# Kernel tuning notes

Hardware: AMD Instinct MI355X
Metric: run time of the kernel (lower is better)

The kernel has to match this reference:

```python
import jax, jax.numpy as jnp
import numpy as np

N_NODES = 100000


def gcn_conv(x, edge_index, W, b, num_nodes):
    """PyG GCNConv: y = D^{-1/2} (A + I) D^{-1/2} (x W) + b.

    edge_index[0] = source (row), edge_index[1] = target (col);
    messages flow source -> target with symmetric normalization.
    """
    # add self loops
    loop = jnp.arange(num_nodes, dtype=edge_index.dtype)
    row = jnp.concatenate([edge_index[0], loop])  # [E+N]
    col = jnp.concatenate([edge_index[1], loop])  # [E+N]

    xw = x @ W  # [N, F_out] -- tiny GEMM, done before gather

    # degree of target nodes (incl. self loops)
    ones = jnp.ones(col.shape[0], dtype=x.dtype)
    deg = jax.ops.segment_sum(ones, col, num_segments=num_nodes)  # [N]
    dis = jax.lax.rsqrt(jnp.maximum(deg, 1e-12))
    dis = jnp.where(deg > 0, dis, 0.0)

    norm = dis[row] * dis[col]  # [E+N]
    msg = xw[row] * norm[:, None]  # gather + scale, [E+N, F_out]
    out = jax.ops.segment_sum(msg, col, num_segments=num_nodes)  # scatter-add
    return out + b


def setup_inputs() -> dict:
    key = jax.random.key(0)
    k1, k2, k3, k4 = jax.random.split(key, 4)
    num_attr, hidden, num_classes = 128, 16, 8
    n_edges = 3200000
    x = jax.random.normal(k1, (N_NODES, num_attr), dtype=jnp.float32)
    edge_index = jax.random.randint(k2, (2, n_edges), 0, N_NODES, dtype=jnp.int64)
    W1 = jax.random.normal(k3, (num_attr, hidden), dtype=jnp.float32) / np.sqrt(num_attr)
    b1 = jnp.zeros((hidden,), dtype=jnp.float32)
    W2 = jax.random.normal(k4, (hidden, num_classes), dtype=jnp.float32) / np.sqrt(hidden)
    b2 = jnp.zeros((num_classes,), dtype=jnp.float32)
    return {"x": x, "edge_index": edge_index, "W1": W1, "b1": b1, "W2": W2, "b2": b2}


def reference(x, edge_index, W1, b1, W2, b2):
    h = gcn_conv(x, edge_index, W1, b1, N_NODES)
    h = jax.nn.relu(h)
    # dropout is identity in eval mode
    h = gcn_conv(h, edge_index, W2, b2, N_NODES)
    return jax.nn.sigmoid(h)  # [N, num_classes]
```

## Files before the change

kernel.cpp:

```cpp
#include <hip/hip_runtime.h>
#include <math.h>

static constexpr int FI = 128;
static constexpr int FH = 16;
static constexpr int FO = 8;

static constexpr int BIN_SHIFT = 10;
static constexpr int BIN_NODES = 1024;
static constexpr int MAX_BINS  = 128;
static constexpr int CAPB      = 35328;
static constexpr int SCHUNK    = 4096;
static constexpr int SThreads  = 512;

__device__ __forceinline__ unsigned short f2bf(float x) {
    unsigned u = __float_as_uint(x);
    u += 0x7FFFu + ((u >> 16) & 1u);
    return (unsigned short)(u >> 16);
}
__device__ __forceinline__ float bf2f(unsigned short h) {
    return __uint_as_float((unsigned)h << 16);
}
__device__ __forceinline__ float bflo(unsigned u) { return __uint_as_float(u << 16); }
__device__ __forceinline__ float bfhi(unsigned u) { return __uint_as_float(u & 0xFFFF0000u); }

__global__ void k_initcur(int* __restrict__ binCursor, int nbins) {
    int i = threadIdx.x;
    if (i < nbins) binCursor[i] = i * CAPB;
}

__launch_bounds__(SThreads)
__global__ void k_binscatter(const int* __restrict__ row, const int* __restrict__ col,
                             int* __restrict__ binCursor, unsigned int* __restrict__ binned,
                             int E, int nbins) {
    __shared__ int lcnt[MAX_BINS];
    __shared__ int lsc[MAX_BINS];
    __shared__ int lstart[MAX_BINS];
    __shared__ int lcur[MAX_BINS];
    __shared__ int gbase[MAX_BINS];
    __shared__ unsigned int  staged[SCHUNK];
    __shared__ unsigned char sbin[SCHUNK];
    int t = threadIdx.x;
    int base = blockIdx.x * SCHUNK;
    int end  = base + SCHUNK; if (end > E) end = E;
    int m = end - base;
    if (t < MAX_BINS) lcnt[t] = 0;
    __syncthreads();

    int nv = m >> 2;
    const int4* c4 = (const int4*)(col + base);
    for (int k = t; k < nv; k += SThreads) {
        int4 c = c4[k];
        atomicAdd(&lcnt[c.x >> BIN_SHIFT], 1);
        atomicAdd(&lcnt[c.y >> BIN_SHIFT], 1);
        atomicAdd(&lcnt[c.z >> BIN_SHIFT], 1);
        atomicAdd(&lcnt[c.w >> BIN_SHIFT], 1);
    }
    for (int i = base + (nv << 2) + t; i < end; i += SThreads)
        atomicAdd(&lcnt[col[i] >> BIN_SHIFT], 1);
    __syncthreads();

    int v = 0;
    if (t < MAX_BINS) { v = lcnt[t]; lsc[t] = v; }
    __syncthreads();
    for (int off = 1; off < MAX_BINS; off <<= 1) {
        int x = (t >= off && t < MAX_BINS) ? lsc[t - off] : 0;
        __syncthreads();
        if (t < MAX_BINS) lsc[t] += x;
        __syncthreads();
    }
    if (t < MAX_BINS) {
        int ex = lsc[t] - v;
        lstart[t] = ex;
        lcur[t]   = ex;
        gbase[t]  = v ? atomicAdd(&binCursor[t], v) : 0;
    }
    __syncthreads();

    const int4* r4 = (const int4*)(row + base);
    for (int k = t; k < nv; k += SThreads) {
        int4 c = c4[k]; int4 r = r4[k];
        int cc[4] = {c.x, c.y, c.z, c.w};
        int rr[4] = {r.x, r.y, r.z, r.w};
        #pragma unroll
        for (int j = 0; j < 4; ++j) {
            int b = cc[j] >> BIN_SHIFT;
            int pos = atomicAdd(&lcur[b], 1);
            staged[pos] = (unsigned)rr[j] | ((unsigned)(cc[j] & (BIN_NODES - 1)) << 17);
            sbin[pos] = (unsigned char)b;
        }
    }
    for (int i = base + (nv << 2) + t; i < end; i += SThreads) {
        int c = col[i];
        int b = c >> BIN_SHIFT;
        int pos = atomicAdd(&lcur[b], 1);
        staged[pos] = (unsigned)row[i] | ((unsigned)(c & (BIN_NODES - 1)) << 17);
        sbin[pos] = (unsigned char)b;
    }
    __syncthreads();

    for (int i = t; i < m; i += SThreads) {
        int b = sbin[i];
        int g = gbase[b] + (i - lstart[b]);
        if (g < (b + 1) * CAPB) binned[g] = staged[i];
    }
}

__launch_bounds__(1024)
__global__ void k_refine(const int* __restrict__ binCursor, const unsigned int* __restrict__ binned,
                         int* __restrict__ srow, int* __restrict__ starts, int* __restrict__ ends,
                         float* __restrict__ dis, int N) {
    __shared__ int cnt[BIN_NODES];
    __shared__ int ls[BIN_NODES];
    int t = threadIdx.x;
    int b = blockIdx.x;
    int s = b * CAPB;
    int m = binCursor[b] - s;
    if (m > CAPB) m = CAPB;
    cnt[t] = 0;
    __syncthreads();

    int mm = m & ~3;
    for (int i0 = t * 4; i0 < mm; i0 += 4096) {
        uint4 v = *(const uint4*)(binned + s + i0);
        atomicAdd(&cnt[v.x >> 17], 1);
        atomicAdd(&cnt[v.y >> 17], 1);
        atomicAdd(&cnt[v.z >> 17], 1);
        atomicAdd(&cnt[v.w >> 17], 1);
    }
    for (int i = mm + t; i < m; i += 1024)
        atomicAdd(&cnt[binned[s + i] >> 17], 1);
    __syncthreads();

    int deg = cnt[t];
    ls[t] = deg;
    __syncthreads();
    for (int off = 1; off < 1024; off <<= 1) {
        int x = (t >= off) ? ls[t - off] : 0;
        __syncthreads();
        ls[t] += x;
        __syncthreads();
    }
    int excl = ls[t] - deg;

    int n = b * BIN_NODES + t;
    if (n < N) {
        starts[n] = s + excl;
        ends[n]   = s + excl + deg;
        dis[n]    = rsqrtf((float)(deg + 1));
    }
    cnt[t] = excl;
    __syncthreads();

    for (int i0 = t * 4; i0 < mm; i0 += 4096) {
        uint4 v = *(const uint4*)(binned + s + i0);
        int p0 = atomicAdd(&cnt[v.x >> 17], 1); srow[s + p0] = v.x & 0x1FFFF;
        int p1 = atomicAdd(&cnt[v.y >> 17], 1); srow[s + p1] = v.y & 0x1FFFF;
        int p2 = atomicAdd(&cnt[v.z >> 17], 1); srow[s + p2] = v.z & 0x1FFFF;
        int p3 = atomicAdd(&cnt[v.w >> 17], 1); srow[s + p3] = v.w & 0x1FFFF;
    }
    for (int i = mm + t; i < m; i += 1024) {
        unsigned v = binned[s + i];
        int p = atomicAdd(&cnt[v >> 17], 1);
        srow[s + p] = v & 0x1FFFF;
    }
}

__launch_bounds__(256)
__global__ void k_gemm1(const float* __restrict__ x, const float* __restrict__ W,
                        const float* __restrict__ dis, unsigned short* __restrict__ xw1s,
                        int N) {
    __shared__ float sw[FI * FH];
    int t = threadIdx.x;
    for (int i = t; i < FI * FH; i += 256) sw[i] = W[i];
    __syncthreads();

    int nl = t >> 2;
    int f  = (t & 3) * 4;
    int n  = blockIdx.x * 64 + nl;
    if (n >= N) return;

    const float4* xr = (const float4*)(x + (size_t)n * FI);
    float a0 = 0.f, a1 = 0.f, a2 = 0.f, a3 = 0.f;
    #pragma unroll 8
    for (int kq = 0; kq < FI / 4; ++kq) {
        float4 xv = xr[kq];
        float4 w0 = *(const float4*)&sw[(kq * 4 + 0) * FH + f];
        float4 w1 = *(const float4*)&sw[(kq * 4 + 1) * FH + f];
        float4 w2 = *(const float4*)&sw[(kq * 4 + 2) * FH + f];
        float4 w3 = *(const float4*)&sw[(kq * 4 + 3) * FH + f];
        a0 = fmaf(xv.x, w0.x, a0); a1 = fmaf(xv.x, w0.y, a1);
        a2 = fmaf(xv.x, w0.z, a2); a3 = fmaf(xv.x, w0.w, a3);
        a0 = fmaf(xv.y, w1.x, a0); a1 = fmaf(xv.y, w1.y, a1);
        a2 = fmaf(xv.y, w1.z, a2); a3 = fmaf(xv.y, w1.w, a3);
        a0 = fmaf(xv.z, w2.x, a0); a1 = fmaf(xv.z, w2.y, a1);
        a2 = fmaf(xv.z, w2.z, a2); a3 = fmaf(xv.z, w2.w, a3);
        a0 = fmaf(xv.w, w3.x, a0); a1 = fmaf(xv.w, w3.y, a1);
        a2 = fmaf(xv.w, w3.z, a2); a3 = fmaf(xv.w, w3.w, a3);
    }
    float dn = dis[n];
    unsigned w0 = (unsigned)f2bf(a0 * dn) | ((unsigned)f2bf(a1 * dn) << 16);
    unsigned w1 = (unsigned)f2bf(a2 * dn) | ((unsigned)f2bf(a3 * dn) << 16);
    *(uint2*)(xw1s + (size_t)n * FH + f) = make_uint2(w0, w1);
}

__launch_bounds__(256)
__global__ void k_agg1(const int* __restrict__ starts, const int* __restrict__ ends,
                       const int* __restrict__ srow, const float* __restrict__ dis,
                       const unsigned short* __restrict__ xw1s, const float* __restrict__ W2,
                       const float* __restrict__ b1, unsigned short* __restrict__ xw2s, int N) {
    __shared__ float h1[64][FH + 1];
    __shared__ float sw[FH * FO];
    __shared__ float sb[FH];
    int t = threadIdx.x;
    if (t < FH * FO) sw[t] = W2[t];
    if (t < FH) sb[t] = b1[t];
    int nl = t >> 2;
    int q  = t & 3;
    int n  = blockIdx.x * 64 + nl;
    float dn = 0.f;
    if (n < N) {
        dn = dis[n];
        int s = starts[n], e = ends[n];
        const uint2* xq = (const uint2*)(xw1s) + q;
        uint2 selfpk = xq[(size_t)n * 4];
        float a0 = bflo(selfpk.x), a1 = bfhi(selfpk.x);
        float a2 = bflo(selfpk.y), a3 = bfhi(selfpk.y);
        int i = s;
        for (; i + 8 <= e; i += 8) {
            int rr[8];
            #pragma unroll
            for (int j = 0; j < 8; ++j) rr[j] = srow[i + j];
            uint2 pk[8];
            #pragma unroll
            for (int j = 0; j < 8; ++j) pk[j] = xq[(size_t)rr[j] * 4];
            #pragma unroll
            for (int j = 0; j < 8; ++j) {
                a0 += bflo(pk[j].x); a1 += bfhi(pk[j].x);
                a2 += bflo(pk[j].y); a3 += bfhi(pk[j].y);
            }
        }
        for (; i < e; ++i) {
            uint2 p = xq[(size_t)srow[i] * 4];
            a0 += bflo(p.x); a1 += bfhi(p.x);
            a2 += bflo(p.y); a3 += bfhi(p.y);
        }
        int f0 = q * 4;
        float v0 = fmaf(dn, a0, sb[f0 + 0]);
        float v1 = fmaf(dn, a1, sb[f0 + 1]);
        float v2 = fmaf(dn, a2, sb[f0 + 2]);
        float v3 = fmaf(dn, a3, sb[f0 + 3]);
        h1[nl][f0 + 0] = v0 > 0.f ? v0 : 0.f;
        h1[nl][f0 + 1] = v1 > 0.f ? v1 : 0.f;
        h1[nl][f0 + 2] = v2 > 0.f ? v2 : 0.f;
        h1[nl][f0 + 3] = v3 > 0.f ? v3 : 0.f;
    }
    __syncthreads();
    if (n < N) {
        int o0 = q * 2;
        float aL = 0.f, aH = 0.f;
        #pragma unroll
        for (int k = 0; k < FH; ++k) {
            float hv = h1[nl][k];
            aL = fmaf(hv, sw[k * FO + o0],     aL);
            aH = fmaf(hv, sw[k * FO + o0 + 1], aH);
        }
        unsigned pk = (unsigned)f2bf(aL * dn) | ((unsigned)f2bf(aH * dn) << 16);
        *(unsigned*)(xw2s + (size_t)n * FO + o0) = pk;
    }
}

__launch_bounds__(256)
__global__ void k_agg2(const int* __restrict__ starts, const int* __restrict__ ends,
                       const int* __restrict__ srow, const float* __restrict__ dis,
                       const unsigned short* __restrict__ xw2s, const float* __restrict__ b2,
                       float* __restrict__ out, int N) {
    int t = threadIdx.x;
    int nl = t >> 1;
    int h  = t & 1;
    int n  = blockIdx.x * 128 + nl;
    if (n >= N) return;
    float dn = dis[n];
    int s = starts[n], e = ends[n];
    const uint2* xq = (const uint2*)(xw2s) + h;
    uint2 selfpk = xq[(size_t)n * 2];
    float a0 = bflo(selfpk.x), a1 = bfhi(selfpk.x);
    float a2 = bflo(selfpk.y), a3 = bfhi(selfpk.y);
    int i = s;
    for (; i + 8 <= e; i += 8) {
        int rr[8];
        #pragma unroll
        for (int j = 0; j < 8; ++j) rr[j] = srow[i + j];
        uint2 pk[8];
        #pragma unroll
        for (int j = 0; j < 8; ++j) pk[j] = xq[(size_t)rr[j] * 2];
        #pragma unroll
        for (int j = 0; j < 8; ++j) {
            a0 += bflo(pk[j].x); a1 += bfhi(pk[j].x);
            a2 += bflo(pk[j].y); a3 += bfhi(pk[j].y);
        }
    }
    for (; i < e; ++i) {
        uint2 p = xq[(size_t)srow[i] * 2];
        a0 += bflo(p.x); a1 += bfhi(p.x);
        a2 += bflo(p.y); a3 += bfhi(p.y);
    }
    int f0 = h * 4;
    float v0 = fmaf(dn, a0, b2[f0 + 0]);
    float v1 = fmaf(dn, a1, b2[f0 + 1]);
    float v2 = fmaf(dn, a2, b2[f0 + 2]);
    float v3 = fmaf(dn, a3, b2[f0 + 3]);
    float4 r = make_float4(1.f / (1.f + __expf(-v0)), 1.f / (1.f + __expf(-v1)),
                           1.f / (1.f + __expf(-v2)), 1.f / (1.f + __expf(-v3)));
    *(float4*)(out + (size_t)n * FO + f0) = r;
}

extern "C" void kernel_launch(void* const* d_in, const int* in_sizes, int n_in,
                              void* d_out, int out_size, void* d_ws, size_t ws_size,
                              hipStream_t stream) {
    const float* x  = (const float*)d_in[0];
    const int*   ei = (const int*)d_in[1];
    const float* W1 = (const float*)d_in[2];
    const float* b1 = (const float*)d_in[3];
    const float* W2 = (const float*)d_in[4];
    const float* b2 = (const float*)d_in[5];

    const int N = in_sizes[0] / FI;
    const int E = in_sizes[1] / 2;
    const int* row = ei;
    const int* col = ei + E;
    const int nbins = (N + BIN_NODES - 1) >> BIN_SHIFT;

    const size_t NP = 100352;
    const size_t BINSZ = (size_t)nbins * CAPB;
    float* base = (float*)d_ws;
    int*   starts    = (int*)base;
    int*   ends      = (int*)(base + NP);
    float* dis       = base + 2 * NP;
    int*   binCursor = (int*)(base + 3 * NP);
    unsigned int* binned = (unsigned int*)(base + 3 * NP + 1024);
    int*   srow      = (int*)(base + 3 * NP + 1024 + BINSZ);
    unsigned short* xw1s = (unsigned short*)binned;
    unsigned short* xw2s = (unsigned short*)(base + 3 * NP + 1024 + NP * 8);
    float* out = (float*)d_out;

    size_t needed = (3 * NP + 1024 + 2 * BINSZ) * 4;
    if (ws_size < needed) return;

    k_initcur   <<<1, 128,                               0, stream>>>(binCursor, nbins);
    k_binscatter<<<(E + SCHUNK - 1) / SCHUNK, SThreads,  0, stream>>>(row, col, binCursor, binned, E, nbins);
    k_refine    <<<nbins, 1024,                          0, stream>>>(binCursor, binned, srow, starts, ends, dis, N);
    k_gemm1     <<<(N + 63) / 64, 256,                   0, stream>>>(x, W1, dis, xw1s, N);
    k_agg1      <<<(N + 63) / 64, 256,                   0, stream>>>(starts, ends, srow, dis, xw1s, W2, b1, xw2s, N);
    k_agg2      <<<(N + 127) / 128, 256,                 0, stream>>>(starts, ends, srow, dis, xw2s, b2, out, N);
}
```

Measured before the change: 134.6 us.

## Use one thread per node in aggregation kernels and wave-shuffle scan in refine

Both aggregation kernels now assign a whole node to a single thread, which loads the full bf16 feature row with 16-byte vector loads instead of splitting features across 2-4 threads. This cuts the repeated index loads and the shared-memory transpose for the second GEMM, at the cost of more registers and fewer threads per node for latency hiding. The refine kernel's 10-step shared-memory prefix scan becomes a wave-level shuffle scan plus a small cross-wave pass. The binscatter chunk size is also doubled.

```diff
diff --git a/kernel.cpp b/kernel.cpp
--- a/kernel.cpp
+++ b/kernel.cpp
@@ -9,16 +9,13 @@
 static constexpr int BIN_NODES = 1024;
 static constexpr int MAX_BINS  = 128;
 static constexpr int CAPB      = 35328;
-static constexpr int SCHUNK    = 4096;
+static constexpr int SCHUNK    = 8192;
 static constexpr int SThreads  = 512;
 
 __device__ __forceinline__ unsigned short f2bf(float x) {
     unsigned u = __float_as_uint(x);
     u += 0x7FFFu + ((u >> 16) & 1u);
     return (unsigned short)(u >> 16);
-}
-__device__ __forceinline__ float bf2f(unsigned short h) {
-    return __uint_as_float((unsigned)h << 16);
 }
 __device__ __forceinline__ float bflo(unsigned u) { return __uint_as_float(u << 16); }
 __device__ __forceinline__ float bfhi(unsigned u) { return __uint_as_float(u & 0xFFFF0000u); }
@@ -110,7 +107,7 @@
                          int* __restrict__ srow, int* __restrict__ starts, int* __restrict__ ends,
                          float* __restrict__ dis, int N) {
     __shared__ int cnt[BIN_NODES];
-    __shared__ int ls[BIN_NODES];
+    __shared__ int wsum[16];
     int t = threadIdx.x;
     int b = blockIdx.x;
     int s = b * CAPB;
@@ -132,15 +129,26 @@
     __syncthreads();
 
     int deg = cnt[t];
-    ls[t] = deg;
-    __syncthreads();
-    for (int off = 1; off < 1024; off <<= 1) {
-        int x = (t >= off) ? ls[t - off] : 0;
-        __syncthreads();
-        ls[t] += x;
-        __syncthreads();
-    }
-    int excl = ls[t] - deg;
+    int inc = deg;
+    #pragma unroll
+    for (int d = 1; d < 64; d <<= 1) {
+        int u = __shfl_up(inc, d, 64);
+        if ((t & 63) >= d) inc += u;
+    }
+    if ((t & 63) == 63) wsum[t >> 6] = inc;
+    __syncthreads();
+    if (t < 16) {
+        int w = wsum[t];
+        #pragma unroll
+        for (int d = 1; d < 16; d <<= 1) {
+            int u = __shfl_up(w, d, 16);
+            if (t >= d) w += u;
+        }
+        wsum[t] = w;
+    }
+    __syncthreads();
+    int waveoff = (t >= 64) ? wsum[(t >> 6) - 1] : 0;
+    int excl = waveoff + inc - deg;
 
     int n = b * BIN_NODES + t;
     if (n < N) {
@@ -208,65 +216,80 @@
                        const int* __restrict__ srow, const float* __restrict__ dis,
                        const unsigned short* __restrict__ xw1s, const float* __restrict__ W2,
                        const float* __restrict__ b1, unsigned short* __restrict__ xw2s, int N) {
-    __shared__ float h1[64][FH + 1];
     __shared__ float sw[FH * FO];
     __shared__ float sb[FH];
     int t = threadIdx.x;
     if (t < FH * FO) sw[t] = W2[t];
     if (t < FH) sb[t] = b1[t];
-    int nl = t >> 2;
-    int q  = t & 3;
-    int n  = blockIdx.x * 64 + nl;
-    float dn = 0.f;
-    if (n < N) {
-        dn = dis[n];
-        int s = starts[n], e = ends[n];
-        const uint2* xq = (const uint2*)(xw1s) + q;
-        uint2 selfpk = xq[(size_t)n * 4];
-        float a0 = bflo(selfpk.x), a1 = bfhi(selfpk.x);
-        float a2 = bflo(selfpk.y), a3 = bfhi(selfpk.y);
-        int i = s;
-        for (; i + 8 <= e; i += 8) {
-            int rr[8];
-            #pragma unroll
-            for (int j = 0; j < 8; ++j) rr[j] = srow[i + j];
-            uint2 pk[8];
-            #pragma unroll
-            for (int j = 0; j < 8; ++j) pk[j] = xq[(size_t)rr[j] * 4];
-            #pragma unroll
-            for (int j = 0; j < 8; ++j) {
-                a0 += bflo(pk[j].x); a1 += bfhi(pk[j].x);
-                a2 += bflo(pk[j].y); a3 += bfhi(pk[j].y);
-            }
-        }
-        for (; i < e; ++i) {
-            uint2 p = xq[(size_t)srow[i] * 4];
-            a0 += bflo(p.x); a1 += bfhi(p.x);
-            a2 += bflo(p.y); a3 += bfhi(p.y);
-        }
-        int f0 = q * 4;
-        float v0 = fmaf(dn, a0, sb[f0 + 0]);
-        float v1 = fmaf(dn, a1, sb[f0 + 1]);
-        float v2 = fmaf(dn, a2, sb[f0 + 2]);
-        float v3 = fmaf(dn, a3, sb[f0 + 3]);
-        h1[nl][f0 + 0] = v0 > 0.f ? v0 : 0.f;
-        h1[nl][f0 + 1] = v1 > 0.f ? v1 : 0.f;
-        h1[nl][f0 + 2] = v2 > 0.f ? v2 : 0.f;
-        h1[nl][f0 + 3] = v3 > 0.f ? v3 : 0.f;
-    }
-    __syncthreads();
-    if (n < N) {
-        int o0 = q * 2;
+    __syncthreads();
+
+    int n = blockIdx.x * 256 + t;
+    if (n >= N) return;
+    float dn = dis[n];
+    int s = starts[n], e = ends[n];
+    const uint4* xq = (const uint4*)xw1s;
+
+    uint4 s0 = xq[(size_t)n * 2], s1 = xq[(size_t)n * 2 + 1];
+    float acc[16];
+    acc[0]=bflo(s0.x); acc[1]=bfhi(s0.x); acc[2]=bflo(s0.y); acc[3]=bfhi(s0.y);
+    acc[4]=bflo(s0.z); acc[5]=bfhi(s0.z); acc[6]=bflo(s0.w); acc[7]=bfhi(s0.w);
+    acc[8]=bflo(s1.x); acc[9]=bfhi(s1.x); acc[10]=bflo(s1.y); acc[11]=bfhi(s1.y);
+    acc[12]=bflo(s1.z); acc[13]=bfhi(s1.z); acc[14]=bflo(s1.w); acc[15]=bfhi(s1.w);
+
+    int i = s;
+    for (; i + 8 <= e; i += 8) {
+        int rr[8];
+        #pragma unroll
+        for (int j = 0; j < 8; ++j) rr[j] = srow[i + j];
+        uint4 pa[8], pb[8];
+        #pragma unroll
+        for (int j = 0; j < 8; ++j) {
+            pa[j] = xq[(size_t)rr[j] * 2];
+            pb[j] = xq[(size_t)rr[j] * 2 + 1];
+        }
+        #pragma unroll
+        for (int j = 0; j < 8; ++j) {
+            acc[0]+=bflo(pa[j].x);  acc[1]+=bfhi(pa[j].x);
+            acc[2]+=bflo(pa[j].y);  acc[3]+=bfhi(pa[j].y);
+            acc[4]+=bflo(pa[j].z);  acc[5]+=bfhi(pa[j].z);
+            acc[6]+=bflo(pa[j].w);  acc[7]+=bfhi(pa[j].w);
+            acc[8]+=bflo(pb[j].x);  acc[9]+=bfhi(pb[j].x);
+            acc[10]+=bflo(pb[j].y); acc[11]+=bfhi(pb[j].y);
+            acc[12]+=bflo(pb[j].z); acc[13]+=bfhi(pb[j].z);
+            acc[14]+=bflo(pb[j].w); acc[15]+=bfhi(pb[j].w);
+        }
+    }
+    for (; i < e; ++i) {
+        int r = srow[i];
+        uint4 qa = xq[(size_t)r * 2], qb = xq[(size_t)r * 2 + 1];
+        acc[0]+=bflo(qa.x);  acc[1]+=bfhi(qa.x);
+        acc[2]+=bflo(qa.y);  acc[3]+=bfhi(qa.y);
+        acc[4]+=bflo(qa.z);  acc[5]+=bfhi(qa.z);
+        acc[6]+=bflo(qa.w);  acc[7]+=bfhi(qa.w);
+        acc[8]+=bflo(qb.x);  acc[9]+=bfhi(qb.x);
+        acc[10]+=bflo(qb.y); acc[11]+=bfhi(qb.y);
+        acc[12]+=bflo(qb.z); acc[13]+=bfhi(qb.z);
+        acc[14]+=bflo(qb.w); acc[15]+=bfhi(qb.w);
+    }
+
+    float hv[FH];
+    #pragma unroll
+    for (int k = 0; k < FH; ++k) {
+        float v = fmaf(dn, acc[k], sb[k]);
+        hv[k] = v > 0.f ? v : 0.f;
+    }
+    unsigned o[4];
+    #pragma unroll
+    for (int p = 0; p < 4; ++p) {
         float aL = 0.f, aH = 0.f;
         #pragma unroll
         for (int k = 0; k < FH; ++k) {
-            float hv = h1[nl][k];
-            aL = fmaf(hv, sw[k * FO + o0],     aL);
-            aH = fmaf(hv, sw[k * FO + o0 + 1], aH);
-        }
-        unsigned pk = (unsigned)f2bf(aL * dn) | ((unsigned)f2bf(aH * dn) << 16);
-        *(unsigned*)(xw2s + (size_t)n * FO + o0) = pk;
-    }
+            aL = fmaf(hv[k], sw[k * FO + 2 * p],     aL);
+            aH = fmaf(hv[k], sw[k * FO + 2 * p + 1], aH);
+        }
+        o[p] = (unsigned)f2bf(aL * dn) | ((unsigned)f2bf(aH * dn) << 16);
+    }
+    *(uint4*)(xw2s + (size_t)n * FO) = make_uint4(o[0], o[1], o[2], o[3]);
 }
 
 __launch_bounds__(256)
@@ -275,43 +298,49 @@
                        const unsigned short* __restrict__ xw2s, const float* __restrict__ b2,
                        float* __restrict__ out, int N) {
     int t = threadIdx.x;
-    int nl = t >> 1;
-    int h  = t & 1;
-    int n  = blockIdx.x * 128 + nl;
+    int n = blockIdx.x * 256 + t;
     if (n >= N) return;
     float dn = dis[n];
     int s = starts[n], e = ends[n];
-    const uint2* xq = (const uint2*)(xw2s) + h;
-    uint2 selfpk = xq[(size_t)n * 2];
-    float a0 = bflo(selfpk.x), a1 = bfhi(selfpk.x);
-    float a2 = bflo(selfpk.y), a3 = bfhi(selfpk.y);
+    const uint4* xq = (const uint4*)xw2s;
+
+    uint4 sp = xq[n];
+    float acc[8];
+    acc[0]=bflo(sp.x); acc[1]=bfhi(sp.x); acc[2]=bflo(sp.y); acc[3]=bfhi(sp.y);
+    acc[4]=bflo(sp.z); acc[5]=bfhi(sp.z); acc[6]=bflo(sp.w); acc[7]=bfhi(sp.w);
+
     int i = s;
     for (; i + 8 <= e; i += 8) {
         int rr[8];
         #pragma unroll
         for (int j = 0; j < 8; ++j) rr[j] = srow[i + j];
-        uint2 pk[8];
-        #pragma unroll
-        for (int j = 0; j < 8; ++j) pk[j] = xq[(size_t)rr[j] * 2];
+        uint4 pk[8];
+        #pragma unroll
+        for (int j = 0; j < 8; ++j) pk[j] = xq[rr[j]];
         #pragma unroll
         for (int j = 0; j < 8; ++j) {
-            a0 += bflo(pk[j].x); a1 += bfhi(pk[j].x);
-            a2 += bflo(pk[j].y); a3 += bfhi(pk[j].y);
+            acc[0]+=bflo(pk[j].x); acc[1]+=bfhi(pk[j].x);
+            acc[2]+=bflo(pk[j].y); acc[3]+=bfhi(pk[j].y);
+            acc[4]+=bflo(pk[j].z); acc[5]+=bfhi(pk[j].z);
+            acc[6]+=bflo(pk[j].w); acc[7]+=bfhi(pk[j].w);
         }
     }
     for (; i < e; ++i) {
-        uint2 p = xq[(size_t)srow[i] * 2];
-        a0 += bflo(p.x); a1 += bfhi(p.x);
-        a2 += bflo(p.y); a3 += bfhi(p.y);
-    }
-    int f0 = h * 4;
-    float v0 = fmaf(dn, a0, b2[f0 + 0]);
-    float v1 = fmaf(dn, a1, b2[f0 + 1]);
-    float v2 = fmaf(dn, a2, b2[f0 + 2]);
-    float v3 = fmaf(dn, a3, b2[f0 + 3]);
-    float4 r = make_float4(1.f / (1.f + __expf(-v0)), 1.f / (1.f + __expf(-v1)),
-                           1.f / (1.f + __expf(-v2)), 1.f / (1.f + __expf(-v3)));
-    *(float4*)(out + (size_t)n * FO + f0) = r;
+        uint4 p = xq[srow[i]];
+        acc[0]+=bflo(p.x); acc[1]+=bfhi(p.x);
+        acc[2]+=bflo(p.y); acc[3]+=bfhi(p.y);
+        acc[4]+=bflo(p.z); acc[5]+=bfhi(p.z);
+        acc[6]+=bflo(p.w); acc[7]+=bfhi(p.w);
+    }
+
+    float r[FO];
+    #pragma unroll
+    for (int k = 0; k < FO; ++k) {
+        float v = fmaf(dn, acc[k], b2[k]);
+        r[k] = 1.f / (1.f + __expf(-v));
+    }
+    *(float4*)(out + (size_t)n * FO)     = make_float4(r[0], r[1], r[2], r[3]);
+    *(float4*)(out + (size_t)n * FO + 4) = make_float4(r[4], r[5], r[6], r[7]);
 }
 
 extern "C" void kernel_launch(void* const* d_in, const int* in_sizes, int n_in,
@@ -350,6 +379,6 @@
     k_binscatter<<<(E + SCHUNK - 1) / SCHUNK, SThreads,  0, stream>>>(row, col, binCursor, binned, E, nbins);
     k_refine    <<<nbins, 1024,                          0, stream>>>(binCursor, binned, srow, starts, ends, dis, N);
     k_gemm1     <<<(N + 63) / 64, 256,                   0, stream>>>(x, W1, dis, xw1s, N);
-    k_agg1      <<<(N + 63) / 64, 256,                   0, stream>>>(starts, ends, srow, dis, xw1s, W2, b1, xw2s, N);
-    k_agg2      <<<(N + 127) / 128, 256,                 0, stream>>>(starts, ends, srow, dis, xw2s, b2, out, N);
-}
+    k_agg1      <<<(N + 255) / 256, 256,                 0, stream>>>(starts, ends, srow, dis, xw1s, W2, b1, xw2s, N);
+    k_agg2      <<<(N + 255) / 256, 256,                 0, stream>>>(starts, ends, srow, dis, xw2s, b2, out, N);
+}
```

Result: faster. 130.8 us (-2.9%).
